# Kernel tuning notes

Hardware: AMD Instinct MI355X
Metric: run time of the kernel (lower is better)

## Reference

```python
import jax, jax.numpy as jnp
import numpy as np


def _sepconv1x1(x, dw, pw, b):
    # SeparableConv2D with kernel=1: depthwise 1x1 = per-channel scale, then pointwise matmul
    return jnp.einsum('nhwc,cd->nhwd', x * dw, pw) + b


def setup_inputs() -> dict:
    key = jax.random.key(0)
    ks = jax.random.split(key, 12)
    N, H, W, C_in, C_red = 4, 64, 64, 256, 64
    s = 0.05  # small init so softmax logits are well-conditioned
    return {
        'feature_maps': jax.random.normal(ks[0], (N, H, W, C_in), jnp.float32),
        'global_channel_output': jax.random.normal(ks[1], (N, H, W, C_in), jnp.float32),
        'dw_q': jax.random.normal(ks[2], (C_in,), jnp.float32) * s,
        'pw_q': jax.random.normal(ks[3], (C_in, C_red), jnp.float32) * s,
        'b_q': jnp.zeros((C_red,), jnp.float32),
        'dw_k': jax.random.normal(ks[4], (C_in,), jnp.float32) * s,
        'pw_k': jax.random.normal(ks[5], (C_in, C_red), jnp.float32) * s,
        'b_k': jnp.zeros((C_red,), jnp.float32),
        'dw_v': jax.random.normal(ks[6], (C_in,), jnp.float32) * s,
        'pw_v': jax.random.normal(ks[7], (C_in, C_red), jnp.float32) * s,
        'b_v': jnp.zeros((C_red,), jnp.float32),
        'dw_a': jax.random.normal(ks[8], (C_red,), jnp.float32) * s,
        'pw_a': jax.random.normal(ks[9], (C_red, C_in), jnp.float32) * s,
        'b_a': jnp.zeros((C_in,), jnp.float32),
    }


def reference(feature_maps, global_channel_output,
              dw_q, pw_q, b_q, dw_k, pw_k, b_k, dw_v, pw_v, b_v,
              dw_a, pw_a, b_a):
    N, H, W, _ = feature_maps.shape
    q = _sepconv1x1(feature_maps, dw_q, pw_q, b_q)  # [N,H,W,Cr]
    k = _sepconv1x1(feature_maps, dw_k, pw_k, b_k)
    v = _sepconv1x1(feature_maps, dw_v, pw_v, b_v)
    Cr = q.shape[-1]
    q = q.reshape(N, H * W, Cr)
    k = k.reshape(N, H * W, Cr)
    v = v.reshape(N, H * W, Cr)
    # tf.matmul(key, query, transpose_b=True): scores[i,j] = key_i . query_j
    scores = jnp.einsum('nic,njc->nij', k, q)  # [N,HW,HW]
    scores = jax.nn.softmax(scores, axis=-1)
    # tf.matmul(value, scores, transpose_a=True) -> [N,Cr,HW]
    att = jnp.einsum('nic,nij->ncj', v, scores)
    # faithful raw reshape (as in the original TF code) from [N,Cr,HW] to [N,H,W,Cr]
    att = att.reshape(N, H, W, Cr)
    att = _sepconv1x1(att, dw_a, pw_a, b_a)  # [N,H,W,C_in]
    return global_channel_output * att + global_channel_output
```

## Files before the change

### kernel.cpp

```cpp
#include <hip/hip_runtime.h>
#include <hip/hip_bf16.h>

typedef __attribute__((ext_vector_type(8))) __bf16 bf16x8;
typedef __attribute__((ext_vector_type(2))) __bf16 bf16x2;
typedef __attribute__((ext_vector_type(4))) float floatx4;
typedef __attribute__((ext_vector_type(4))) unsigned short us4;
typedef __attribute__((ext_vector_type(8))) unsigned short us8;
typedef __attribute__((ext_vector_type(4))) short s16x4;
typedef __attribute__((ext_vector_type(2))) unsigned int uint2v;
typedef __attribute__((ext_vector_type(4))) unsigned int uint4v;

#define MFMA16(A, B, C) __builtin_amdgcn_mfma_f32_16x16x32_bf16((A), (B), (C), 0, 0, 0)
#define MFMA1K(A, B, C) __builtin_amdgcn_mfma_f32_16x16x16bf16_1k((A), (B), (C), 0, 0, 0)

#define LOG2E 1.44269504088896340736f

#if __has_builtin(__builtin_amdgcn_exp2f)
#define EXP2F(x) __builtin_amdgcn_exp2f(x)
#else
#define EXP2F(x) exp2f(x)
#endif

static __device__ __forceinline__ unsigned short f2bfbits(float f) {
    __hip_bfloat16 h = __float2bfloat16(f);
    union { __hip_bfloat16 h; unsigned short u; } cv;
    cv.h = h;
    return cv.u;
}
static __device__ __forceinline__ unsigned int rne32(float f) {
    unsigned int u = __builtin_bit_cast(unsigned int, f);
    return u + 0x7fffu + ((u >> 16) & 1u);
}
static __device__ __forceinline__ unsigned short rne16(float f) {
    return (unsigned short)(rne32(f) >> 16);
}

#if __has_builtin(__builtin_amdgcn_cvt_pk_bf16_f32)
static __device__ __forceinline__ s16x4 pack4(float e0, float e1, float e2, float e3) {
    bf16x2 lo = __builtin_amdgcn_cvt_pk_bf16_f32(e0, e1);
    bf16x2 hi = __builtin_amdgcn_cvt_pk_bf16_f32(e2, e3);
    uint2v u = {__builtin_bit_cast(unsigned int, lo), __builtin_bit_cast(unsigned int, hi)};
    return __builtin_bit_cast(s16x4, u);
}
static __device__ __forceinline__ bf16x8 cvt8(floatx4 a, floatx4 b) {
    bf16x2 p0 = __builtin_amdgcn_cvt_pk_bf16_f32(a[0], a[1]);
    bf16x2 p1 = __builtin_amdgcn_cvt_pk_bf16_f32(a[2], a[3]);
    bf16x2 p2 = __builtin_amdgcn_cvt_pk_bf16_f32(b[0], b[1]);
    bf16x2 p3 = __builtin_amdgcn_cvt_pk_bf16_f32(b[2], b[3]);
    uint4v u = {__builtin_bit_cast(unsigned int, p0), __builtin_bit_cast(unsigned int, p1),
                __builtin_bit_cast(unsigned int, p2), __builtin_bit_cast(unsigned int, p3)};
    return __builtin_bit_cast(bf16x8, u);
}
#else
static __device__ __forceinline__ s16x4 pack4(float e0, float e1, float e2, float e3) {
    unsigned int pa = __builtin_amdgcn_perm(rne32(e1), rne32(e0), 0x07060302u);
    unsigned int pb = __builtin_amdgcn_perm(rne32(e3), rne32(e2), 0x07060302u);
    uint2v u = {pa, pb};
    return __builtin_bit_cast(s16x4, u);
}
static __device__ __forceinline__ bf16x8 cvt8(floatx4 a, floatx4 b) {
    us8 u;
#pragma unroll
    for (int i = 0; i < 4; i++) { u[i] = rne16(a[i]); u[4 + i] = rne16(b[i]); }
    return __builtin_bit_cast(bf16x8, u);
}
#endif

static __device__ __forceinline__ bf16x8 load_bf8(const __hip_bfloat16* p) {
    return *reinterpret_cast<const bf16x8*>(p);
}
static __device__ __forceinline__ float bf2f(unsigned short u) {
    unsigned int w = ((unsigned int)u) << 16;
    return __builtin_bit_cast(float, w);
}


__global__ __launch_bounds__(256) void proj_qkv(
    const float* __restrict__ x,
    const float* __restrict__ dwq, const float* __restrict__ pwq,
    const float* __restrict__ dwk, const float* __restrict__ pwk,
    const float* __restrict__ dwv, const float* __restrict__ pwv,
    const float* __restrict__ bqp, const float* __restrict__ bkp,
    const float* __restrict__ bvp,
    __hip_bfloat16* __restrict__ qf, __hip_bfloat16* __restrict__ kf,
    __hip_bfloat16* __restrict__ vf)
{
    __shared__ __hip_bfloat16 wle[16384];
    int b = blockIdx.x;
    int p = b >> 8;
    int tg = b & 255;
    int tid = threadIdx.x;

    const float* dw = (p == 0) ? dwq : ((p == 1) ? dwk : dwv);
    const float* pw = (p == 0) ? pwq : ((p == 1) ? pwk : pwv);
    float scale = (p == 1) ? LOG2E : 1.0f;

    {
        float dwc = dw[tid];
#pragma unroll
        for (int k = 0; k < 64; k++) {
            int idx = (k * 256 + tid) ^ ((k & 7) << 3);
            wle[idx] = __float2bfloat16(dwc * pw[tid * 64 + k] * scale);
        }
    }
    __syncthreads();

    int wv = tid >> 6;
    int wid = tg * 4 + wv;
    int lane = tid & 63;
    int l15 = lane & 15, quad = lane >> 4;

    floatx4 acc[4];
#pragma unroll
    for (int t = 0; t < 4; t++) acc[t] = (floatx4){0.f, 0.f, 0.f, 0.f};

    const float* xrow = x + (wid * 16 + l15) * 256 + quad * 8;
#pragma unroll
    for (int ks = 0; ks < 8; ks++) {
        floatx4 xa = *reinterpret_cast<const floatx4*>(xrow + ks * 32);
        floatx4 xb = *reinterpret_cast<const floatx4*>(xrow + ks * 32 + 4);
        bf16x8 a = cvt8(xa, xb);
#pragma unroll
        for (int t = 0; t < 4; t++) {
            int j0 = ((t * 16 + l15) * 256 + ks * 32 + quad * 8) ^ ((l15 & 7) << 3);
            bf16x8 bfr = *reinterpret_cast<const bf16x8*>(&wle[j0]);
            acc[t] = MFMA16(a, bfr, acc[t]);
        }
    }
    if (p < 2) {
        __hip_bfloat16* dst = (p == 0) ? qf : kf;
        const float* bias = (p == 0) ? bqp : bkp;
        float bscale = (p == 1) ? LOG2E : 1.0f;
#pragma unroll
        for (int t = 0; t < 4; t++) {
            float bsv = bias[t * 16 + l15] * bscale;
            int off0 = wid * 1024 + (t >> 1) * 512 +
                       (((((t & 1) << 1) | (l15 >> 3)) * 16 + quad * 4) * 8) + (l15 & 7);
#pragma unroll
            for (int r = 0; r < 4; r++)
                dst[off0 + r * 8] = __float2bfloat16(acc[t][r] + bsv);
        }
    } else {
#pragma unroll
        for (int t = 0; t < 4; t++) {
            float bsv = bvp[t * 16 + l15];
            us4 pk;
#pragma unroll
            for (int r = 0; r < 4; r++) pk[r] = f2bfbits(acc[t][r] + bsv);
            *reinterpret_cast<us4*>(vf + (wid * 4 + t) * 256 + lane * 4) = pk;
        }
    }
}

#define P1STEP(B0, B1, B2, B3) do {                                        \
    floatx4 z = (floatx4){0.f, 0.f, 0.f, 0.f};                             \
    floatx4 sA0 = MFMA16(a1, (B1), MFMA16(a0, (B0), z));                   \
    floatx4 sA1 = MFMA16(a1, (B3), MFMA16(a0, (B2), z));                   \
    floatx4 sB0 = MFMA16(a3, (B1), MFMA16(a2, (B0), z));                   \
    floatx4 sB1 = MFMA16(a3, (B3), MFMA16(a2, (B2), z));                   \
    _Pragma("unroll")                                                      \
    for (int r = 0; r < 4; r++) {                                          \
        lsA[r] += EXP2F(sA0[r]) + EXP2F(sA1[r]);                           \
        lsB[r] += EXP2F(sB0[r]) + EXP2F(sB1[r]);                           \
    }                                                                      \
} while (0)

__global__ __launch_bounds__(512) void pass1_rl(
    const __hip_bfloat16* __restrict__ qf, const __hip_bfloat16* __restrict__ kf,
    const __hip_bfloat16* __restrict__ vf, __hip_bfloat16* __restrict__ vfs)
{
    int itg0 = blockIdx.x * 2;
    int n = itg0 >> 8;
    int jw = threadIdx.x >> 6;
    int lane = threadIdx.x & 63;
    int l15 = lane & 15, quad = lane >> 4;

    const __hip_bfloat16* kp = kf + itg0 * 1024 + lane * 8;
    bf16x8 a0 = load_bf8(kp);
    bf16x8 a1 = load_bf8(kp + 512);
    bf16x8 a2 = load_bf8(kp + 1024);
    bf16x8 a3 = load_bf8(kp + 1536);

    floatx4 lsA = (floatx4){0.f, 0.f, 0.f, 0.f};
    floatx4 lsB = (floatx4){0.f, 0.f, 0.f, 0.f};
    const __hip_bfloat16* qp0 = qf + (n * 256 + jw * 32) * 1024 + lane * 8;

    bf16x8 s0b0 = load_bf8(qp0);
    bf16x8 s0b1 = load_bf8(qp0 + 512);
    bf16x8 s0b2 = load_bf8(qp0 + 1024);
    bf16x8 s0b3 = load_bf8(qp0 + 1536);
    bf16x8 s1b0 = load_bf8(qp0 + 2048);
    bf16x8 s1b1 = load_bf8(qp0 + 2560);
    bf16x8 s1b2 = load_bf8(qp0 + 3072);
    bf16x8 s1b3 = load_bf8(qp0 + 3584);

    for (int it = 0; it < 16; it += 2) {
        bf16x8 n0 = load_bf8(qp0 + 4096);
        bf16x8 n1 = load_bf8(qp0 + 4608);
        bf16x8 n2 = load_bf8(qp0 + 5120);
        bf16x8 n3 = load_bf8(qp0 + 5632);
        P1STEP(s0b0, s0b1, s0b2, s0b3);
        s0b0 = n0; s0b1 = n1; s0b2 = n2; s0b3 = n3;
        bf16x8 m0 = load_bf8(qp0 + 6144);
        bf16x8 m1 = load_bf8(qp0 + 6656);
        bf16x8 m2 = load_bf8(qp0 + 7168);
        bf16x8 m3 = load_bf8(qp0 + 7680);
        P1STEP(s1b0, s1b1, s1b2, s1b3);
        s1b0 = m0; s1b1 = m1; s1b2 = m2; s1b3 = m3;
        qp0 += 4096;
    }
#pragma unroll
    for (int m = 1; m < 16; m <<= 1) {
#pragma unroll
        for (int r = 0; r < 4; r++) {
            lsA[r] += __shfl_xor(lsA[r], m, 64);
            lsB[r] += __shfl_xor(lsB[r], m, 64);
        }
    }
    __shared__ float red[8][32];
    __shared__ float rls[32];
    if (l15 == 0) {
#pragma unroll
        for (int r = 0; r < 4; r++) {
            red[jw][quad * 4 + r] = lsA[r];
            red[jw][16 + quad * 4 + r] = lsB[r];
        }
    }
    __syncthreads();
    if (threadIdx.x < 32) {
        float tot = 0.f;
#pragma unroll
        for (int w = 0; w < 8; w++) tot += red[w][threadIdx.x];
        rls[threadIdx.x] = 1.0f / tot;
    }
    __syncthreads();
    int m0 = threadIdx.x * 4;
    int toff = m0 >> 10;
    int mm = m0 & 1023;
    int t = mm >> 8;
    int l = (mm >> 2) & 63;
    int rb = toff * 16 + (l >> 4) * 4;
    us4 vv = *reinterpret_cast<const us4*>(
        reinterpret_cast<const unsigned short*>(vf) + itg0 * 1024 + m0);
    us4 ov;
#pragma unroll
    for (int r = 0; r < 4; r++) ov[r] = rne16(bf2f(vv[r]) * rls[rb + r]);
    *reinterpret_cast<us4*>(
        reinterpret_cast<unsigned short*>(vfs) + (itg0 + toff) * 1024 + l * 16 + t * 4) = ov;
}

#define P2STEP(KA, KB, VA, VB) do {                                            \
    floatx4 z = (floatx4){0.f, 0.f, 0.f, 0.f};                                 \
    floatx4 s0 = MFMA16((KB), bq0b, MFMA16((KA), bq0a, z));                    \
    floatx4 s1 = MFMA16((KB), bq1b, MFMA16((KA), bq1a, z));                    \
    floatx4 s2 = MFMA16((KB), bq2b, MFMA16((KA), bq2a, z));                    \
    floatx4 s3 = MFMA16((KB), bq3b, MFMA16((KA), bq3a, z));                    \
    s16x4 p0 = pack4(EXP2F(s0[0]), EXP2F(s0[1]), EXP2F(s0[2]), EXP2F(s0[3])); \
    s16x4 p1 = pack4(EXP2F(s1[0]), EXP2F(s1[1]), EXP2F(s1[2]), EXP2F(s1[3])); \
    s16x4 p2 = pack4(EXP2F(s2[0]), EXP2F(s2[1]), EXP2F(s2[2]), EXP2F(s2[3])); \
    s16x4 p3 = pack4(EXP2F(s3[0]), EXP2F(s3[1]), EXP2F(s3[2]), EXP2F(s3[3])); \
    s16x4 bv0 = __builtin_bit_cast(s16x4, __builtin_shufflevector((VA), (VA), 0, 1, 2, 3)); \
    s16x4 bv1 = __builtin_bit_cast(s16x4, __builtin_shufflevector((VA), (VA), 4, 5, 6, 7)); \
    s16x4 bv2 = __builtin_bit_cast(s16x4, __builtin_shufflevector((VB), (VB), 0, 1, 2, 3)); \
    s16x4 bv3 = __builtin_bit_cast(s16x4, __builtin_shufflevector((VB), (VB), 4, 5, 6, 7)); \
    acc0[0] = MFMA1K(p0, bv0, acc0[0]);                                        \
    acc1[0] = MFMA1K(p1, bv0, acc1[0]);                                        \
    acc2[0] = MFMA1K(p2, bv0, acc2[0]);                                        \
    acc3[0] = MFMA1K(p3, bv0, acc3[0]);                                        \
    acc0[1] = MFMA1K(p0, bv1, acc0[1]);                                        \
    acc1[1] = MFMA1K(p1, bv1, acc1[1]);                                        \
    acc2[1] = MFMA1K(p2, bv1, acc2[1]);                                        \
    acc3[1] = MFMA1K(p3, bv1, acc3[1]);                                        \
    acc0[2] = MFMA1K(p0, bv2, acc0[2]);                                        \
    acc1[2] = MFMA1K(p1, bv2, acc1[2]);                                        \
    acc2[2] = MFMA1K(p2, bv2, acc2[2]);                                        \
    acc3[2] = MFMA1K(p3, bv2, acc3[2]);                                        \
    acc0[3] = MFMA1K(p0, bv3, acc0[3]);                                        \
    acc1[3] = MFMA1K(p1, bv3, acc1[3]);                                        \
    acc2[3] = MFMA1K(p2, bv3, acc2[3]);                                        \
    acc3[3] = MFMA1K(p3, bv3, acc3[3]);                                        \
} while (0)

__global__ __launch_bounds__(256) void pass2_att(
    const __hip_bfloat16* __restrict__ qf, const __hip_bfloat16* __restrict__ kf,
    const __hip_bfloat16* __restrict__ vfs,
    unsigned short* __restrict__ attp)
{
    int b = blockIdx.x;
    int xcd = b & 7, slot = b >> 3;
    int g = xcd + 8 * (slot >> 4);
    int jg = slot & 15;
    int n = g >> 3, ih = g & 7;
    int w = threadIdx.x >> 6;
    int jt0 = jg * 16 + w * 4;
    int lane = threadIdx.x & 63;
    int l15 = lane & 15, quad = lane >> 4;

    const __hip_bfloat16* qp = qf + (n * 256 + jt0) * 1024 + lane * 8;
    bf16x8 bq0a = load_bf8(qp);
    bf16x8 bq0b = load_bf8(qp + 512);
    bf16x8 bq1a = load_bf8(qp + 1024);
    bf16x8 bq1b = load_bf8(qp + 1536);
    bf16x8 bq2a = load_bf8(qp + 2048);
    bf16x8 bq2b = load_bf8(qp + 2560);
    bf16x8 bq3a = load_bf8(qp + 3072);
    bf16x8 bq3b = load_bf8(qp + 3584);

    floatx4 acc0[4], acc1[4], acc2[4], acc3[4];
#pragma unroll
    for (int t = 0; t < 4; t++) {
        acc0[t] = (floatx4){0.f, 0.f, 0.f, 0.f};
        acc1[t] = (floatx4){0.f, 0.f, 0.f, 0.f};
        acc2[t] = (floatx4){0.f, 0.f, 0.f, 0.f};
        acc3[t] = (floatx4){0.f, 0.f, 0.f, 0.f};
    }

    int it0 = n * 256 + ih * 32;
    const __hip_bfloat16* kp = kf + it0 * 1024 + lane * 8;
    const __hip_bfloat16* vp = vfs + it0 * 1024 + lane * 16;

    bf16x8 kA0 = load_bf8(kp);
    bf16x8 kB0 = load_bf8(kp + 512);
    us8 vA0 = *reinterpret_cast<const us8*>(vp);
    us8 vB0 = *reinterpret_cast<const us8*>(vp + 8);
    bf16x8 kA1 = load_bf8(kp + 1024);
    bf16x8 kB1 = load_bf8(kp + 1536);
    us8 vA1 = *reinterpret_cast<const us8*>(vp + 1024);
    us8 vB1 = *reinterpret_cast<const us8*>(vp + 1024 + 8);

    for (int it = 0; it < 32; it += 2) {
        bf16x8 nkA = load_bf8(kp + 2048);
        bf16x8 nkB = load_bf8(kp + 2560);
        us8 nvA = *reinterpret_cast<const us8*>(vp + 2048);
        us8 nvB = *reinterpret_cast<const us8*>(vp + 2048 + 8);
        P2STEP(kA0, kB0, vA0, vB0);
        kA0 = nkA; kB0 = nkB; vA0 = nvA; vB0 = nvB;
        bf16x8 mkA = load_bf8(kp + 3072);
        bf16x8 mkB = load_bf8(kp + 3584);
        us8 mvA = *reinterpret_cast<const us8*>(vp + 3072);
        us8 mvB = *reinterpret_cast<const us8*>(vp + 3072 + 8);
        P2STEP(kA1, kB1, vA1, vB1);
        kA1 = mkA; kB1 = mkB; vA1 = mvA; vB1 = mvB;
        kp += 2048; vp += 2048;
    }
    unsigned short* op0 = attp + ih * 1048576;
#pragma unroll
    for (int t = 0; t < 4; t++) {
        s16x4 k0 = pack4(acc0[t][0], acc0[t][1], acc0[t][2], acc0[t][3]);
        s16x4 k1 = pack4(acc1[t][0], acc1[t][1], acc1[t][2], acc1[t][3]);
        s16x4 k2 = pack4(acc2[t][0], acc2[t][1], acc2[t][2], acc2[t][3]);
        s16x4 k3 = pack4(acc3[t][0], acc3[t][1], acc3[t][2], acc3[t][3]);
        unsigned short* op = op0 + (n * 64 + t * 16 + l15) * 4096 + jt0 * 16 + quad * 4;
        *reinterpret_cast<s16x4*>(op) = k0;
        *reinterpret_cast<s16x4*>(op + 16) = k1;
        *reinterpret_cast<s16x4*>(op + 32) = k2;
        *reinterpret_cast<s16x4*>(op + 48) = k3;
    }
}

template<int NPART>
__global__ __launch_bounds__(256) void final_out(
    const unsigned short* __restrict__ attp, const float* __restrict__ gco,
    const float* __restrict__ dwa, const float* __restrict__ pwa,
    const float* __restrict__ ba, float* __restrict__ out)
{
    int b = blockIdx.x;
    int n = b >> 9;
    int hh = (b >> 3) & 63;
    int w0 = (b & 7) << 3;
    __shared__ float g[512];
    int tid = threadIdx.x;
    const unsigned short* ap = attp + (n * 64 + hh) * 4096 + w0 * 64;
    {
        int jj0 = tid * 2;
        float v0 = 0.f, v1 = 0.f;
#pragma unroll
        for (int ph = 0; ph < NPART; ph++) {
            unsigned int u = *reinterpret_cast<const unsigned int*>(ap + ph * 1048576 + jj0);
            v0 += bf2f((unsigned short)(u & 0xffffu));
            v1 += bf2f((unsigned short)(u >> 16));
        }
        g[jj0] = v0 * dwa[jj0 & 63];
        g[jj0 + 1] = v1 * dwa[(jj0 + 1) & 63];
    }
    __syncthreads();
    float acc[8];
#pragma unroll
    for (int w = 0; w < 8; w++) acc[w] = 0.f;
    for (int cc = 0; cc < 64; cc++) {
        float p = pwa[cc * 256 + tid];
#pragma unroll
        for (int w = 0; w < 8; w++) acc[w] += g[w * 64 + cc] * p;
    }
    float bb = ba[tid];
#pragma unroll
    for (int w = 0; w < 8; w++) {
        int pos = (n * 64 + hh) * 64 + w0 + w;
        float gv = gco[pos * 256 + tid];
        out[pos * 256 + tid] = gv * (acc[w] + bb) + gv;
    }
}

extern "C" void kernel_launch(void* const* d_in, const int* in_sizes, int n_in,
                              void* d_out, int out_size, void* d_ws, size_t ws_size,
                              hipStream_t stream) {
    const float* x   = (const float*)d_in[0];
    const float* gco = (const float*)d_in[1];
    const float* dwq = (const float*)d_in[2];
    const float* pwq = (const float*)d_in[3];
    const float* bq  = (const float*)d_in[4];
    const float* dwk = (const float*)d_in[5];
    const float* pwk = (const float*)d_in[6];
    const float* bk  = (const float*)d_in[7];
    const float* dwv = (const float*)d_in[8];
    const float* pwv = (const float*)d_in[9];
    const float* bv  = (const float*)d_in[10];
    const float* dwa = (const float*)d_in[11];
    const float* pwa = (const float*)d_in[12];
    const float* ba  = (const float*)d_in[13];
    float* out = (float*)d_out;

    char* ws = (char*)d_ws;
    __hip_bfloat16* qf  = (__hip_bfloat16*)(ws + 98304);
    __hip_bfloat16* kf  = (__hip_bfloat16*)(ws + 2195456);
    __hip_bfloat16* vf  = (__hip_bfloat16*)(ws + 4292608);
    __hip_bfloat16* vfs = (__hip_bfloat16*)(ws + 6389760);
    unsigned short* attp = (unsigned short*)(ws + 8486912);

    proj_qkv<<<768, 256, 0, stream>>>(x, dwq, pwq, dwk, pwk, dwv, pwv,
                                      bq, bk, bv, qf, kf, vf);
    pass1_rl<<<512, 512, 0, stream>>>(qf, kf, vf, vfs);
    pass2_att<<<512, 256, 0, stream>>>(qf, kf, vfs, attp);
    final_out<8><<<2048, 256, 0, stream>>>(attp, gco, dwa, pwa, ba, out);
}
```

Baseline: 169.7 us.

## Stage K/V tiles through LDS with async global_load_lds double buffering in pass2

The attention pass now uses 512-thread blocks that share K and V tiles. Each block loads them cooperatively into a double-buffered LDS ring with global_load_lds, where before every wave streamed K/V from global memory on its own. The V-scaling write in pass1 changes its layout to match the new LDS read pattern. This cuts redundant global and L2 traffic across waves, but adds a barrier every phase and halves the block count.

```diff
diff --git a/kernel.cpp b/kernel.cpp
--- a/kernel.cpp
+++ b/kernel.cpp
@@ -72,6 +72,12 @@
 static __device__ __forceinline__ float bf2f(unsigned short u) {
     unsigned int w = ((unsigned int)u) << 16;
     return __builtin_bit_cast(float, w);
+}
+
+static __device__ __forceinline__ void gld16(const void* g, void* l) {
+    __builtin_amdgcn_global_load_lds(
+        (const __attribute__((address_space(1))) unsigned int*)g,
+        (__attribute__((address_space(3))) unsigned int*)l, 16, 0, 0);
 }
 
 
@@ -245,8 +251,9 @@
     us4 ov;
 #pragma unroll
     for (int r = 0; r < 4; r++) ov[r] = rne16(bf2f(vv[r]) * rls[rb + r]);
+    int oidx = (t >> 1) * 512 + l * 8 + (t & 1) * 4;
     *reinterpret_cast<us4*>(
-        reinterpret_cast<unsigned short*>(vfs) + (itg0 + toff) * 1024 + l * 16 + t * 4) = ov;
+        reinterpret_cast<unsigned short*>(vfs) + (itg0 + toff) * 1024 + oidx) = ov;
 }
 
 #define P2STEP(KA, KB, VA, VB) do {                                            \
@@ -281,20 +288,21 @@
     acc3[3] = MFMA1K(p3, bv3, acc3[3]);                                        \
 } while (0)
 
-__global__ __launch_bounds__(256) void pass2_att(
+__global__ __launch_bounds__(512) void pass2_att(
     const __hip_bfloat16* __restrict__ qf, const __hip_bfloat16* __restrict__ kf,
     const __hip_bfloat16* __restrict__ vfs,
     unsigned short* __restrict__ attp)
 {
+    __shared__ char ldsbuf[2][8192];
     int b = blockIdx.x;
-    int xcd = b & 7, slot = b >> 3;
-    int g = xcd + 8 * (slot >> 4);
-    int jg = slot & 15;
-    int n = g >> 3, ih = g & 7;
-    int w = threadIdx.x >> 6;
-    int jt0 = jg * 16 + w * 4;
-    int lane = threadIdx.x & 63;
+    int ih = b & 7;
+    int jgrp = (b >> 3) & 7;
+    int n = b >> 6;
+    int tid = threadIdx.x;
+    int w = tid >> 6;
+    int lane = tid & 63;
     int l15 = lane & 15, quad = lane >> 4;
+    int jt0 = jgrp * 32 + w * 4;
 
     const __hip_bfloat16* qp = qf + (n * 256 + jt0) * 1024 + lane * 8;
     bf16x8 bq0a = load_bf8(qp);
@@ -316,32 +324,30 @@
     }
 
     int it0 = n * 256 + ih * 32;
-    const __hip_bfloat16* kp = kf + it0 * 1024 + lane * 8;
-    const __hip_bfloat16* vp = vfs + it0 * 1024 + lane * 16;
-
-    bf16x8 kA0 = load_bf8(kp);
-    bf16x8 kB0 = load_bf8(kp + 512);
-    us8 vA0 = *reinterpret_cast<const us8*>(vp);
-    us8 vB0 = *reinterpret_cast<const us8*>(vp + 8);
-    bf16x8 kA1 = load_bf8(kp + 1024);
-    bf16x8 kB1 = load_bf8(kp + 1536);
-    us8 vA1 = *reinterpret_cast<const us8*>(vp + 1024);
-    us8 vB1 = *reinterpret_cast<const us8*>(vp + 1024 + 8);
-
-    for (int it = 0; it < 32; it += 2) {
-        bf16x8 nkA = load_bf8(kp + 2048);
-        bf16x8 nkB = load_bf8(kp + 2560);
-        us8 nvA = *reinterpret_cast<const us8*>(vp + 2048);
-        us8 nvB = *reinterpret_cast<const us8*>(vp + 2048 + 8);
-        P2STEP(kA0, kB0, vA0, vB0);
-        kA0 = nkA; kB0 = nkB; vA0 = nvA; vB0 = nvB;
-        bf16x8 mkA = load_bf8(kp + 3072);
-        bf16x8 mkB = load_bf8(kp + 3584);
-        us8 mvA = *reinterpret_cast<const us8*>(vp + 3072);
-        us8 mvB = *reinterpret_cast<const us8*>(vp + 3072 + 8);
-        P2STEP(kA1, kB1, vA1, vB1);
-        kA1 = mkA; kB1 = mkB; vA1 = mvA; vB1 = mvB;
-        kp += 2048; vp += 2048;
+    const char* gbase = (w < 4) ? (const char*)(kf + it0 * 1024)
+                                : (const char*)(vfs + it0 * 1024);
+    const char* gw = gbase + ((w >> 1) & 1) * 2048 + (w & 1) * 1024 + lane * 16;
+    char* lw0 = &ldsbuf[0][w * 1024];
+    char* lw1 = &ldsbuf[1][w * 1024];
+
+    gld16(gw, lw0);
+    __syncthreads();
+
+    int cur = 0;
+    for (int ph = 0; ph < 16; ph++) {
+        if (ph < 15)
+            gld16(gw + (ph + 1) * 4096, cur ? lw0 : lw1);
+        const char* base = ldsbuf[cur];
+#pragma unroll
+        for (int t = 0; t < 2; t++) {
+            bf16x8 a0 = *reinterpret_cast<const bf16x8*>(base + t * 2048 + lane * 16);
+            bf16x8 a1 = *reinterpret_cast<const bf16x8*>(base + t * 2048 + 1024 + lane * 16);
+            us8 v01 = *reinterpret_cast<const us8*>(base + 4096 + t * 2048 + lane * 16);
+            us8 v23 = *reinterpret_cast<const us8*>(base + 4096 + t * 2048 + 1024 + lane * 16);
+            P2STEP(a0, a1, v01, v23);
+        }
+        __syncthreads();
+        cur ^= 1;
     }
     unsigned short* op0 = attp + ih * 1048576;
 #pragma unroll
@@ -430,6 +436,6 @@
     proj_qkv<<<768, 256, 0, stream>>>(x, dwq, pwq, dwk, pwk, dwv, pwv,
                                       bq, bk, bv, qf, kf, vf);
     pass1_rl<<<512, 512, 0, stream>>>(qf, kf, vf, vfs);
-    pass2_att<<<512, 256, 0, stream>>>(qf, kf, vfs, attp);
+    pass2_att<<<256, 512, 0, stream>>>(qf, kf, vfs, attp);
     final_out<8><<<2048, 256, 0, stream>>>(attp, gco, dwa, pwa, ba, out);
 }
```

Result: faster. 165.7 us (-2.4%).
